# Kernel optimization log

Measured on AMD Instinct MI355X. Metric: run time of the kernel, lower is better.

Reference implementation:

```python
import jax, jax.numpy as jnp
import numpy as np

B, C, W, H = 16, 256, 64, 64
D = C // 8  # query/key head dim = 32


def setup_inputs() -> dict:
    key = jax.random.key(0)
    k1, k2, k3 = jax.random.split(key, 3)
    x = jax.random.normal(k1, (B, C, W, H), dtype=jnp.float32)
    # 1x1 conv weights, squeezed to [out_ch, in_ch]
    Wq = jax.random.normal(k2, (D, C), dtype=jnp.float32) * (1.0 / np.sqrt(C))
    Wk = jax.random.normal(k3, (D, C), dtype=jnp.float32) * (1.0 / np.sqrt(C))
    return {"x": x, "Wq": Wq, "Wk": Wk}


def reference(x, Wq, Wk):
    # x: [B, C, W, H]. Attention is row-restricted: independent per (b, w),
    # attending over the H axis. (value_conv in the torch module is unused.)
    q = jnp.einsum('bcwh,dc->bwhd', x, Wq)          # [B, W, H, D]
    k = jnp.einsum('bcwh,dc->bwdh', x, Wk)          # [B, W, D, H]
    energy = jnp.einsum('bwhd,bwdj->bwhj', q, k)    # [B, W, H, H] (unscaled)
    attn = jax.nn.softmax(energy, axis=-1)          # softmax over keys j
    v = jnp.transpose(x, (0, 2, 1, 3))              # [B, W, C, H]
    # torch: bmm(v, attn^T): out[c, i] = sum_j v[c, j] * attn[i, j]
    out = jnp.einsum('bwcj,bwij->bwci', v, attn)    # [B, W, C, H]
    out = jnp.transpose(out, (0, 2, 1, 3))          # [B, C, W, H]
    return out * x                                  # elementwise gate
```

## Files before the change

kernel.cpp:

```cpp
#include <hip/hip_runtime.h>

#define CCH 256
#define WH 4096

typedef short bf16x8 __attribute__((ext_vector_type(8)));
typedef float f32x4  __attribute__((ext_vector_type(4)));
typedef unsigned u32x4 __attribute__((ext_vector_type(4)));

__device__ __forceinline__ unsigned f2bf(float f) {
  unsigned u = __builtin_bit_cast(unsigned, f);
  u += 0x7fffu + ((u >> 16) & 1u);
  return (u >> 16) & 0xffffu;
}
__device__ __forceinline__ float bf2f(unsigned s) {
  return __builtin_bit_cast(float, s << 16);
}

__device__ __forceinline__ void split2(float f0, float f1, unsigned& hiw, unsigned& low) {
  const unsigned u0 = __builtin_bit_cast(unsigned, f0);
  const unsigned u1 = __builtin_bit_cast(unsigned, f1);
  hiw = (u0 >> 16) | (u1 & 0xFFFF0000u);
  const float h0 = __builtin_bit_cast(float, u0 & 0xFFFF0000u);
  const float h1 = __builtin_bit_cast(float, u1 & 0xFFFF0000u);
  low = f2bf(f0 - h0) | (f2bf(f1 - h1) << 16);
}

__global__ __launch_bounds__(256) void wsplit_kernel(
    const float* __restrict__ Wq, const float* __restrict__ Wk,
    short* __restrict__ ws) {
  const int gid    = blockIdx.x * 256 + threadIdx.x;
  const int fragid = gid >> 6;
  const int lane   = gid & 63;
  const int mt = fragid & 3;
  const int kt = fragid >> 2;
  const int dp = mt * 16 + (lane & 15);
  const int cb = kt * 32 + ((lane >> 4) & 3) * 8;
  const float* Wrow = (dp < 32) ? (Wq + (size_t)dp * CCH)
                                : (Wk + (size_t)(dp - 32) * CCH);
  bf16x8 hfr, lfr;
  #pragma unroll
  for (int t = 0; t < 8; ++t) {
    const float v = Wrow[cb + t];
    const unsigned h = f2bf(v);
    hfr[t] = (short)h;
    lfr[t] = (short)f2bf(v - bf2f(h));
  }
  *(bf16x8*)(ws + (size_t)gid * 8)         = hfr;
  *(bf16x8*)(ws + 16384 + (size_t)gid * 8) = lfr;
}

__global__ __launch_bounds__(256)
__attribute__((amdgpu_waves_per_eu(4, 4)))
void selfattn_kernel(
    const float* __restrict__ x, const short* __restrict__ ws,
    float* __restrict__ out) {
  __shared__ float    q_lds[32 * 64];
  __shared__ float    k_lds[64 * 36];
  __shared__ unsigned attn32[8 * 8 * 64];
  __shared__ float    red1[4 * 64];
  __shared__ float    red2[4 * 64];

  const int tid  = threadIdx.x;
  const int lane = tid & 63;
  const int wave = tid >> 6;
  const int g    = lane >> 4;
  const int r16  = lane & 15;
  const int blk  = blockIdx.x;
  const int b    = blk >> 6;
  const int w    = blk & 63;

  const float* xb = x   + (size_t)b * CCH * WH + (size_t)w * 64;
  float*       ob = out + (size_t)b * CCH * WH + (size_t)w * 64;

  {
    const int col = wave * 16 + r16;
    f32x4 acc[4] = {{0,0,0,0},{0,0,0,0},{0,0,0,0},{0,0,0,0}};
    #pragma unroll
    for (int kt = 0; kt < 8; ++kt) {
      float xs[8];
      #pragma unroll
      for (int t = 0; t < 8; ++t)
        xs[t] = xb[(size_t)(kt*32 + g*8 + t) * WH + col];
      unsigned hw[4], lw[4];
      #pragma unroll
      for (int r = 0; r < 4; ++r) split2(xs[2*r], xs[2*r+1], hw[r], lw[r]);
      const bf16x8 xbh = __builtin_bit_cast(bf16x8, (u32x4){hw[0],hw[1],hw[2],hw[3]});
      const bf16x8 xbl = __builtin_bit_cast(bf16x8, (u32x4){lw[0],lw[1],lw[2],lw[3]});
      #pragma unroll
      for (int mt = 0; mt < 4; ++mt) {
        const bf16x8 ah = *(const bf16x8*)(ws + (size_t)((kt*4 + mt)*64 + lane) * 8);
        const bf16x8 al = *(const bf16x8*)(ws + 16384 + (size_t)((kt*4 + mt)*64 + lane) * 8);
        acc[mt] = __builtin_amdgcn_mfma_f32_16x16x32_bf16(ah, xbh, acc[mt], 0, 0, 0);
        acc[mt] = __builtin_amdgcn_mfma_f32_16x16x32_bf16(ah, xbl, acc[mt], 0, 0, 0);
        acc[mt] = __builtin_amdgcn_mfma_f32_16x16x32_bf16(al, xbh, acc[mt], 0, 0, 0);
      }
    }
    #pragma unroll
    for (int mt = 0; mt < 2; ++mt)
      #pragma unroll
      for (int r = 0; r < 4; ++r)
        q_lds[(mt*16 + g*4 + r) * 64 + col] = acc[mt][r];
    #pragma unroll
    for (int mt = 2; mt < 4; ++mt)
      #pragma unroll
      for (int r = 0; r < 4; ++r)
        k_lds[col * 36 + (mt-2)*16 + g*4 + r] = acc[mt][r];
  }
  __syncthreads();

  float qreg[32];
  #pragma unroll
  for (int d = 0; d < 32; ++d) qreg[d] = q_lds[d * 64 + lane];

  float e[16];
  #pragma unroll
  for (int jj = 0; jj < 16; ++jj) {
    const float4* kr = (const float4*)&k_lds[(wave*16 + jj) * 36];
    float acc = 0.f;
    #pragma unroll
    for (int d4 = 0; d4 < 8; ++d4) {
      const float4 kv = kr[d4];
      acc += qreg[4*d4+0]*kv.x + qreg[4*d4+1]*kv.y
           + qreg[4*d4+2]*kv.z + qreg[4*d4+3]*kv.w;
    }
    e[jj] = acc;
  }
  float pm = e[0];
  #pragma unroll
  for (int jj = 1; jj < 16; ++jj) pm = fmaxf(pm, e[jj]);
  red1[wave*64 + lane] = pm;
  __syncthreads();
  const float m = fmaxf(fmaxf(red1[lane], red1[64 + lane]),
                        fmaxf(red1[128 + lane], red1[192 + lane]));
  float s = 0.f;
  #pragma unroll
  for (int jj = 0; jj < 16; ++jj) { e[jj] = __expf(e[jj] - m); s += e[jj]; }
  red2[wave*64 + lane] = s;
  __syncthreads();
  const float stot = (red2[lane] + red2[64 + lane]) + (red2[128 + lane] + red2[192 + lane]);
  const float rs = 1.0f / stot;
  {
    const int fbase = (lane >> 4) * 2 + (wave >> 1);
    #pragma unroll
    for (int jj = 0; jj < 16; ++jj) {
      const float p = e[jj] * rs;
      const unsigned u = __builtin_bit_cast(unsigned, p);
      const float hif = __builtin_bit_cast(float, u & 0xFFFF0000u);
      const unsigned lo = f2bf(p - hif);
      const int l2 = (((wave & 1) * 2 + (jj >> 3)) << 4) | r16;
      attn32[fbase*512 + (jj & 7)*64 + l2] = (u >> 16) | (lo << 16);
    }
  }
  __syncthreads();

  const int c0w = wave * 64;
  #pragma unroll
  for (int half = 0; half < 2; ++half) {
    bf16x8 bh[2][2], bl[2][2];
    #pragma unroll
    for (int itl = 0; itl < 2; ++itl)
      #pragma unroll
      for (int ks = 0; ks < 2; ++ks) {
        const int f = (half*2 + itl)*2 + ks;
        unsigned wv[8];
        #pragma unroll
        for (int t = 0; t < 8; ++t) wv[t] = attn32[f*512 + t*64 + lane];
        u32x4 hwv, lwv;
        #pragma unroll
        for (int r = 0; r < 4; ++r) {
          hwv[r] = (wv[2*r] & 0xFFFFu) | (wv[2*r+1] << 16);
          lwv[r] = (wv[2*r] >> 16)     | (wv[2*r+1] & 0xFFFF0000u);
        }
        bh[itl][ks] = __builtin_bit_cast(bf16x8, hwv);
        bl[itl][ks] = __builtin_bit_cast(bf16x8, lwv);
      }
    #pragma unroll
    for (int ct = 0; ct < 4; ++ct) {
      const int crow = c0w + ct*16 + r16;
      const float4* xrow = (const float4*)(xb + (size_t)crow * WH);
      bf16x8 xh[2], xl[2];
      #pragma unroll
      for (int ks = 0; ks < 2; ++ks) {
        const float4 fa = xrow[ks*8 + g*2];
        const float4 fb = xrow[ks*8 + g*2 + 1];
        unsigned hw[4], lw[4];
        split2(fa.x, fa.y, hw[0], lw[0]);
        split2(fa.z, fa.w, hw[1], lw[1]);
        split2(fb.x, fb.y, hw[2], lw[2]);
        split2(fb.z, fb.w, hw[3], lw[3]);
        xh[ks] = __builtin_bit_cast(bf16x8, (u32x4){hw[0],hw[1],hw[2],hw[3]});
        xl[ks] = __builtin_bit_cast(bf16x8, (u32x4){lw[0],lw[1],lw[2],lw[3]});
      }
      #pragma unroll
      for (int itl = 0; itl < 2; ++itl) {
        f32x4 acc = {0.f, 0.f, 0.f, 0.f};
        #pragma unroll
        for (int ks = 0; ks < 2; ++ks) {
          acc = __builtin_amdgcn_mfma_f32_16x16x32_bf16(xh[ks], bh[itl][ks], acc, 0, 0, 0);
          acc = __builtin_amdgcn_mfma_f32_16x16x32_bf16(xh[ks], bl[itl][ks], acc, 0, 0, 0);
          acc = __builtin_amdgcn_mfma_f32_16x16x32_bf16(xl[ks], bh[itl][ks], acc, 0, 0, 0);
        }
        const int i = (half*2 + itl)*16 + r16;
        #pragma unroll
        for (int r = 0; r < 4; ++r) {
          const int c = c0w + ct*16 + g*4 + r;
          const float xg = xb[(size_t)c * WH + i];
          ob[(size_t)c * WH + i] = acc[r] * xg;
        }
      }
    }
  }
}

extern "C" void kernel_launch(void* const* d_in, const int* in_sizes, int n_in,
                              void* d_out, int out_size, void* d_ws, size_t ws_size,
                              hipStream_t stream) {
  (void)in_sizes; (void)n_in; (void)out_size; (void)ws_size;
  const float* x  = (const float*)d_in[0];
  const float* Wq = (const float*)d_in[1];
  const float* Wk = (const float*)d_in[2];
  float* out = (float*)d_out;
  hipLaunchKernelGGL(wsplit_kernel, dim3(8), dim3(256), 0, stream,
                     Wq, Wk, (short*)d_ws);
  hipLaunchKernelGGL(selfattn_kernel, dim3(16 * 64), dim3(256), 0, stream,
                     x, (const short*)d_ws, out);
}
```

Measured before the change: 163.2 us.

## Split fused attention kernel into QK-softmax and PV-gate kernels via workspace

Splits the single fused kernel into two launches. The first computes Q/K projections and the softmax, then writes the packed bf16 hi/lo attention matrix to global workspace. The second reloads it into LDS and does the PV product and gate. The aim is lower register and LDS pressure per kernel for higher occupancy, at the cost of a 16 MB global round trip and an extra launch. The fused path stays as a fallback, now without the waves_per_eu attribute, for when the workspace is too small.

Result: slower. 170.3 us (+4.4%).

```diff
diff --git a/kernel.cpp b/kernel.cpp
--- a/kernel.cpp
+++ b/kernel.cpp
@@ -49,16 +49,13 @@
   *(bf16x8*)(ws + 16384 + (size_t)gid * 8) = lfr;
 }
 
-__global__ __launch_bounds__(256)
-__attribute__((amdgpu_waves_per_eu(4, 4)))
-void selfattn_kernel(
+__global__ __launch_bounds__(256) void qk_softmax_kernel(
     const float* __restrict__ x, const short* __restrict__ ws,
-    float* __restrict__ out) {
-  __shared__ float    q_lds[32 * 64];
-  __shared__ float    k_lds[64 * 36];
-  __shared__ unsigned attn32[8 * 8 * 64];
-  __shared__ float    red1[4 * 64];
-  __shared__ float    red2[4 * 64];
+    unsigned* __restrict__ attnG) {
+  __shared__ float q_lds[32 * 64];
+  __shared__ float k_lds[64 * 36];
+  __shared__ float red1[4 * 64];
+  __shared__ float red2[4 * 64];
 
   const int tid  = threadIdx.x;
   const int lane = tid & 63;
@@ -69,8 +66,7 @@
   const int b    = blk >> 6;
   const int w    = blk & 63;
 
-  const float* xb = x   + (size_t)b * CCH * WH + (size_t)w * 64;
-  float*       ob = out + (size_t)b * CCH * WH + (size_t)w * 64;
+  const float* xb = x + (size_t)b * CCH * WH + (size_t)w * 64;
 
   {
     const int col = wave * 16 + r16;
@@ -140,7 +136,8 @@
   const float stot = (red2[lane] + red2[64 + lane]) + (red2[128 + lane] + red2[192 + lane]);
   const float rs = 1.0f / stot;
   {
-    const int fbase = (lane >> 4) * 2 + (wave >> 1);
+    unsigned* aB = attnG + (size_t)blk * 4096;
+    const int fbase = g * 2 + (wave >> 1);
     #pragma unroll
     for (int jj = 0; jj < 16; ++jj) {
       const float p = e[jj] * rs;
@@ -148,7 +145,34 @@
       const float hif = __builtin_bit_cast(float, u & 0xFFFF0000u);
       const unsigned lo = f2bf(p - hif);
       const int l2 = (((wave & 1) * 2 + (jj >> 3)) << 4) | r16;
-      attn32[fbase*512 + (jj & 7)*64 + l2] = (u >> 16) | (lo << 16);
+      aB[fbase*512 + (jj & 7)*64 + l2] = (u >> 16) | (lo << 16);
+    }
+  }
+}
+
+__global__ __launch_bounds__(256) void pv_gate_kernel(
+    const float* __restrict__ x, const unsigned* __restrict__ attnG,
+    float* __restrict__ out) {
+  __shared__ unsigned attnL[4096];
+
+  const int tid  = threadIdx.x;
+  const int lane = tid & 63;
+  const int wave = tid >> 6;
+  const int g    = lane >> 4;
+  const int r16  = lane & 15;
+  const int blk  = blockIdx.x;
+  const int b    = blk >> 6;
+  const int w    = blk & 63;
+
+  const float* xb = x   + (size_t)b * CCH * WH + (size_t)w * 64;
+  float*       ob = out + (size_t)b * CCH * WH + (size_t)w * 64;
+
+  {
+    const unsigned* aB = attnG + (size_t)blk * 4096;
+    #pragma unroll
+    for (int q = 0; q < 4; ++q) {
+      const int idx = q * 1024 + tid * 4;
+      *(u32x4*)&attnL[idx] = *(const u32x4*)&aB[idx];
     }
   }
   __syncthreads();
@@ -164,7 +188,7 @@
         const int f = (half*2 + itl)*2 + ks;
         unsigned wv[8];
         #pragma unroll
-        for (int t = 0; t < 8; ++t) wv[t] = attn32[f*512 + t*64 + lane];
+        for (int t = 0; t < 8; ++t) wv[t] = attnL[f*512 + t*64 + lane];
         u32x4 hwv, lwv;
         #pragma unroll
         for (int r = 0; r < 4; ++r) {
@@ -212,16 +236,188 @@
   }
 }
 
+__global__ __launch_bounds__(256) void selfattn_fused(
+    const float* __restrict__ x, const short* __restrict__ ws,
+    float* __restrict__ out) {
+  __shared__ float    q_lds[32 * 64];
+  __shared__ float    k_lds[64 * 36];
+  __shared__ unsigned attn32[4096];
+  __shared__ float    red1[4 * 64];
+  __shared__ float    red2[4 * 64];
+
+  const int tid  = threadIdx.x;
+  const int lane = tid & 63;
+  const int wave = tid >> 6;
+  const int g    = lane >> 4;
+  const int r16  = lane & 15;
+  const int blk  = blockIdx.x;
+  const int b    = blk >> 6;
+  const int w    = blk & 63;
+
+  const float* xb = x   + (size_t)b * CCH * WH + (size_t)w * 64;
+  float*       ob = out + (size_t)b * CCH * WH + (size_t)w * 64;
+
+  {
+    const int col = wave * 16 + r16;
+    f32x4 acc[4] = {{0,0,0,0},{0,0,0,0},{0,0,0,0},{0,0,0,0}};
+    #pragma unroll
+    for (int kt = 0; kt < 8; ++kt) {
+      float xs[8];
+      #pragma unroll
+      for (int t = 0; t < 8; ++t)
+        xs[t] = xb[(size_t)(kt*32 + g*8 + t) * WH + col];
+      unsigned hw[4], lw[4];
+      #pragma unroll
+      for (int r = 0; r < 4; ++r) split2(xs[2*r], xs[2*r+1], hw[r], lw[r]);
+      const bf16x8 xbh = __builtin_bit_cast(bf16x8, (u32x4){hw[0],hw[1],hw[2],hw[3]});
+      const bf16x8 xbl = __builtin_bit_cast(bf16x8, (u32x4){lw[0],lw[1],lw[2],lw[3]});
+      #pragma unroll
+      for (int mt = 0; mt < 4; ++mt) {
+        const bf16x8 ah = *(const bf16x8*)(ws + (size_t)((kt*4 + mt)*64 + lane) * 8);
+        const bf16x8 al = *(const bf16x8*)(ws + 16384 + (size_t)((kt*4 + mt)*64 + lane) * 8);
+        acc[mt] = __builtin_amdgcn_mfma_f32_16x16x32_bf16(ah, xbh, acc[mt], 0, 0, 0);
+        acc[mt] = __builtin_amdgcn_mfma_f32_16x16x32_bf16(ah, xbl, acc[mt], 0, 0, 0);
+        acc[mt] = __builtin_amdgcn_mfma_f32_16x16x32_bf16(al, xbh, acc[mt], 0, 0, 0);
+      }
+    }
+    #pragma unroll
+    for (int mt = 0; mt < 2; ++mt)
+      #pragma unroll
+      for (int r = 0; r < 4; ++r)
+        q_lds[(mt*16 + g*4 + r) * 64 + col] = acc[mt][r];
+    #pragma unroll
+    for (int mt = 2; mt < 4; ++mt)
+      #pragma unroll
+      for (int r = 0; r < 4; ++r)
+        k_lds[col * 36 + (mt-2)*16 + g*4 + r] = acc[mt][r];
+  }
+  __syncthreads();
+
+  float qreg[32];
+  #pragma unroll
+  for (int d = 0; d < 32; ++d) qreg[d] = q_lds[d * 64 + lane];
+  float e[16];
+  #pragma unroll
+  for (int jj = 0; jj < 16; ++jj) {
+    const float4* kr = (const float4*)&k_lds[(wave*16 + jj) * 36];
+    float acc = 0.f;
+    #pragma unroll
+    for (int d4 = 0; d4 < 8; ++d4) {
+      const float4 kv = kr[d4];
+      acc += qreg[4*d4+0]*kv.x + qreg[4*d4+1]*kv.y
+           + qreg[4*d4+2]*kv.z + qreg[4*d4+3]*kv.w;
+    }
+    e[jj] = acc;
+  }
+  float pm = e[0];
+  #pragma unroll
+  for (int jj = 1; jj < 16; ++jj) pm = fmaxf(pm, e[jj]);
+  red1[wave*64 + lane] = pm;
+  __syncthreads();
+  const float m = fmaxf(fmaxf(red1[lane], red1[64 + lane]),
+                        fmaxf(red1[128 + lane], red1[192 + lane]));
+  float s = 0.f;
+  #pragma unroll
+  for (int jj = 0; jj < 16; ++jj) { e[jj] = __expf(e[jj] - m); s += e[jj]; }
+  red2[wave*64 + lane] = s;
+  __syncthreads();
+  const float stot = (red2[lane] + red2[64 + lane]) + (red2[128 + lane] + red2[192 + lane]);
+  const float rs = 1.0f / stot;
+  {
+    const int fbase = g * 2 + (wave >> 1);
+    #pragma unroll
+    for (int jj = 0; jj < 16; ++jj) {
+      const float p = e[jj] * rs;
+      const unsigned u = __builtin_bit_cast(unsigned, p);
+      const float hif = __builtin_bit_cast(float, u & 0xFFFF0000u);
+      const unsigned lo = f2bf(p - hif);
+      const int l2 = (((wave & 1) * 2 + (jj >> 3)) << 4) | r16;
+      attn32[fbase*512 + (jj & 7)*64 + l2] = (u >> 16) | (lo << 16);
+    }
+  }
+  __syncthreads();
+
+  const int c0w = wave * 64;
+  #pragma unroll
+  for (int half = 0; half < 2; ++half) {
+    bf16x8 bh[2][2], bl[2][2];
+    #pragma unroll
+    for (int itl = 0; itl < 2; ++itl)
+      #pragma unroll
+      for (int ks = 0; ks < 2; ++ks) {
+        const int f = (half*2 + itl)*2 + ks;
+        unsigned wv[8];
+        #pragma unroll
+        for (int t = 0; t < 8; ++t) wv[t] = attn32[f*512 + t*64 + lane];
+        u32x4 hwv, lwv;
+        #pragma unroll
+        for (int r = 0; r < 4; ++r) {
+          hwv[r] = (wv[2*r] & 0xFFFFu) | (wv[2*r+1] << 16);
+          lwv[r] = (wv[2*r] >> 16)     | (wv[2*r+1] & 0xFFFF0000u);
+        }
+        bh[itl][ks] = __builtin_bit_cast(bf16x8, hwv);
+        bl[itl][ks] = __builtin_bit_cast(bf16x8, lwv);
+      }
+    #pragma unroll
+    for (int ct = 0; ct < 4; ++ct) {
+      const int crow = c0w + ct*16 + r16;
+      const float4* xrow = (const float4*)(xb + (size_t)crow * WH);
+      bf16x8 xh[2], xl[2];
+      #pragma unroll
+      for (int ks = 0; ks < 2; ++ks) {
+        const float4 fa = xrow[ks*8 + g*2];
+        const float4 fb = xrow[ks*8 + g*2 + 1];
+        unsigned hw[4], lw[4];
+        split2(fa.x, fa.y, hw[0], lw[0]);
+        split2(fa.z, fa.w, hw[1], lw[1]);
+        split2(fb.x, fb.y, hw[2], lw[2]);
+        split2(fb.z, fb.w, hw[3], lw[3]);
+        xh[ks] = __builtin_bit_cast(bf16x8, (u32x4){hw[0],hw[1],hw[2],hw[3]});
+        xl[ks] = __builtin_bit_cast(bf16x8, (u32x4){lw[0],lw[1],lw[2],lw[3]});
+      }
+      #pragma unroll
+      for (int itl = 0; itl < 2; ++itl) {
+        f32x4 acc = {0.f, 0.f, 0.f, 0.f};
+        #pragma unroll
+        for (int ks = 0; ks < 2; ++ks) {
+          acc = __builtin_amdgcn_mfma_f32_16x16x32_bf16(xh[ks], bh[itl][ks], acc, 0, 0, 0);
+          acc = __builtin_amdgcn_mfma_f32_16x16x32_bf16(xh[ks], bl[itl][ks], acc, 0, 0, 0);
+          acc = __builtin_amdgcn_mfma_f32_16x16x32_bf16(xl[ks], bh[itl][ks], acc, 0, 0, 0);
+        }
+        const int i = (half*2 + itl)*16 + r16;
+        #pragma unroll
+        for (int r = 0; r < 4; ++r) {
+          const int c = c0w + ct*16 + g*4 + r;
+          const float xg = xb[(size_t)c * WH + i];
+          ob[(size_t)c * WH + i] = acc[r] * xg;
+        }
+      }
+    }
+  }
+}
+
 extern "C" void kernel_launch(void* const* d_in, const int* in_sizes, int n_in,
                               void* d_out, int out_size, void* d_ws, size_t ws_size,
                               hipStream_t stream) {
-  (void)in_sizes; (void)n_in; (void)out_size; (void)ws_size;
+  (void)in_sizes; (void)n_in; (void)out_size;
   const float* x  = (const float*)d_in[0];
   const float* Wq = (const float*)d_in[1];
   const float* Wk = (const float*)d_in[2];
   float* out = (float*)d_out;
+
+  const size_t W_BYTES    = 65536;
+  const size_t ATTN_BYTES = (size_t)1024 * 4096 * 4;
+
   hipLaunchKernelGGL(wsplit_kernel, dim3(8), dim3(256), 0, stream,
                      Wq, Wk, (short*)d_ws);
-  hipLaunchKernelGGL(selfattn_kernel, dim3(16 * 64), dim3(256), 0, stream,
-                     x, (const short*)d_ws, out);
-}
+  if (ws_size >= W_BYTES + ATTN_BYTES) {
+    unsigned* attnG = (unsigned*)((char*)d_ws + W_BYTES);
+    hipLaunchKernelGGL(qk_softmax_kernel, dim3(1024), dim3(256), 0, stream,
+                       x, (const short*)d_ws, attnG);
+    hipLaunchKernelGGL(pv_gate_kernel, dim3(1024), dim3(256), 0, stream,
+                       x, (const unsigned*)attnG, out);
+  } else {
+    hipLaunchKernelGGL(selfattn_fused, dim3(1024), dim3(256), 0, stream,
+                       x, (const short*)d_ws, out);
+  }
+}
```
